# Performance work log

Measured on AMD Instinct MI355X. Metric: run time of the kernel, lower is better.

Reference implementation:

```python
import jax, jax.numpy as jnp
import numpy as np

N_EXPERTS = 64
TOP_K = 4
D_MODEL = 512
D_FF = 2048
B, T = 2, 1024


def setup_inputs() -> dict:
    key = jax.random.key(0)
    k1, k2, k3, k4 = jax.random.split(key, 4)
    x = jax.random.normal(k1, (B, T, D_MODEL), dtype=jnp.float32)
    hex_weights = jax.random.uniform(k2, (B, T, N_EXPERTS), dtype=jnp.float32)
    W_in = jax.random.normal(k3, (N_EXPERTS, D_FF, D_MODEL), dtype=jnp.float32) * (D_MODEL ** -0.5)
    W_out = jax.random.normal(k4, (N_EXPERTS, D_MODEL, D_FF), dtype=jnp.float32) * (D_FF ** -0.5)
    bias_in = jnp.zeros((N_EXPERTS, D_FF), dtype=jnp.float32)
    bias_out = jnp.zeros((N_EXPERTS, D_MODEL), dtype=jnp.float32)
    return {"x": x, "hex_weights": hex_weights, "W_in": W_in, "bias_in": bias_in,
            "W_out": W_out, "bias_out": bias_out}


def reference(x, hex_weights, W_in, bias_in, W_out, bias_out):
    # x: (B,T,D); hex_weights: (B,T,64)
    Bv, Tv, D = x.shape
    N = Bv * Tv
    xf = x.reshape(N, D)
    hw = hex_weights.reshape(N, N_EXPERTS)
    top_w, top_idx = jax.lax.top_k(hw, TOP_K)                 # (N,K)
    top_w = top_w / (jnp.sum(top_w, axis=-1, keepdims=True) + 1e-8)
    # Sparse combine matrix: row n has top_w at selected experts, 0 elsewhere.
    combine = jnp.zeros((N, N_EXPERTS), dtype=x.dtype).at[
        jnp.arange(N)[:, None], top_idx].add(top_w)            # (N,64)
    # Scan over the 64 experts; equivalent math to per-token weight gather,
    # since combine is zero for unselected experts.
    def body(acc, ew):
        Wi, bi, Wo, bo, c = ew                                 # Wi:(d_ff,D), c:(N,)
        h = jax.nn.silu(xf @ Wi.T + bi)                        # (N,d_ff)
        o = h @ Wo.T + bo                                      # (N,D)
        return acc + c[:, None] * o, None
    out, _ = jax.lax.scan(body, jnp.zeros_like(xf),
                          (W_in, bias_in, W_out, bias_out, combine.T))
    return out.reshape(Bv, Tv, D)
```

## Files before the change

kernel.cpp:

```cpp
#include <hip/hip_runtime.h>
#include <hip/hip_bf16.h>
#include <stdint.h>

#define NTOK 2048
#define NE 64
#define TOPK 4
#define DM 512
#define DF 2048
#define TOTSLOT (NTOK*TOPK)

#define BM 192
#define BN 128
#define BK 64
#define GEMM_GRID 1024

typedef __bf16 bf16;
typedef __bf16 bf16x8 __attribute__((ext_vector_type(8)));
typedef __bf16 bf16x4 __attribute__((ext_vector_type(4)));
typedef float  f32x4  __attribute__((ext_vector_type(4)));
typedef short  short8 __attribute__((ext_vector_type(8)));


__global__ void k_route(const float* __restrict__ hw, float* __restrict__ top_w,
                        int* __restrict__ top_idx) {
  int t = blockIdx.x * blockDim.x + threadIdx.x;
  if (t >= NTOK) return;
  const float* r = hw + (size_t)t * NE;
  float rv[NE];
  #pragma unroll
  for (int e = 0; e < NE; ++e) rv[e] = r[e];
  float v[TOPK]; int id[TOPK];
  #pragma unroll
  for (int k = 0; k < TOPK; ++k) {
    float best = -1e30f; int bi = 0;
    #pragma unroll
    for (int e = 0; e < NE; ++e) {
      bool used = false;
      #pragma unroll
      for (int j = 0; j < k; ++j) used |= (id[j] == e);
      if (!used && rv[e] > best) { best = rv[e]; bi = e; }
    }
    v[k] = best; id[k] = bi;
  }
  float den = v[0] + v[1] + v[2] + v[3] + 1e-8f;
  #pragma unroll
  for (int k = 0; k < TOPK; ++k) {
    top_w[t*TOPK + k] = v[k] / den;
    top_idx[t*TOPK + k] = id[k];
  }
}

__global__ __launch_bounds__(256) void k_build(
    const int* __restrict__ top_idx, int* __restrict__ tok,
    int* __restrict__ slot_of, int* __restrict__ offsets_g,
    int* __restrict__ tasklist, int* __restrict__ ntask_g) {
  __shared__ int cnt_s[NE], off_s[NE + 1], fill_s[NE], tpre_s[NE + 1];
  const int tid = threadIdx.x;
  if (tid < NE) { cnt_s[tid] = 0; fill_s[tid] = 0; }
  __syncthreads();
  int ids[TOTSLOT / 256];
  #pragma unroll
  for (int c = 0; c < TOTSLOT / 256; ++c) {
    ids[c] = top_idx[c * 256 + tid];
    atomicAdd(&cnt_s[ids[c]], 1);
  }
  __syncthreads();
  if (tid < 64) {
    int c = cnt_s[tid];
    int inc = c;
    #pragma unroll
    for (int d = 1; d < 64; d <<= 1) {
      int n = __shfl_up(inc, d, 64);
      if (tid >= d) inc += n;
    }
    off_s[tid] = inc - c;
    if (tid == 63) off_s[64] = inc;

    int tc = (c + BM - 1) / BM;
    int tinc = tc;
    #pragma unroll
    for (int d = 1; d < 64; d <<= 1) {
      int n = __shfl_up(tinc, d, 64);
      if (tid >= d) tinc += n;
    }
    tpre_s[tid] = tinc - tc;
    if (tid == 63) tpre_s[64] = tinc;
  }
  __syncthreads();
  #pragma unroll
  for (int c = 0; c < TOTSLOT / 256; ++c) {
    int idx = c * 256 + tid;
    int e = ids[c];
    int pos = off_s[e] + atomicAdd(&fill_s[e], 1);
    tok[pos] = idx >> 2;
    slot_of[idx] = pos;
  }
  if (tid < 64) {
    int tc = (cnt_s[tid] + BM - 1) / BM;
    int base = tpre_s[tid];
    for (int m = 0; m < tc; ++m) tasklist[base + m] = (tid << 8) | m;
    if (tid == 0) *ntask_g = tpre_s[64];
  }
  if (tid <= NE) offsets_g[tid] = off_s[tid];
}

__global__ void k_xcast(const float* __restrict__ x, bf16* __restrict__ xb) {
  int i = blockIdx.x * blockDim.x + threadIdx.x;
  int base = i * 4;
  if (base >= NTOK * DM) return;
  float4 f = *(const float4*)(x + base);
  bf16x4 o;
  o[0] = (bf16)f.x; o[1] = (bf16)f.y; o[2] = (bf16)f.z; o[3] = (bf16)f.w;
  *(bf16x4*)(xb + base) = o;
}


template<int PASS, int KSPLIT>
__global__ __launch_bounds__(512) void k_gemm(
    const float* __restrict__ W, const float* __restrict__ bias,
    const bf16* __restrict__ Asrc, const int* __restrict__ tok,
    const int* __restrict__ offsets,
    const int* __restrict__ tasklist, const int* __restrict__ ntask_g,
    bf16* __restrict__ Hout, float* __restrict__ Oout)
{
  constexpr int KFULL = (PASS == 1) ? DM : DF;
  constexpr int KLOC  = KFULL / KSPLIT;
  constexpr int KT    = KLOC / BK;
  constexpr int NDIM  = (PASS == 1) ? DF : DM;
  constexpr int NT    = NDIM / BN;
  constexpr int NTK   = NT * KSPLIT;

  const int tid = threadIdx.x;
  const int wave = tid >> 6, lane = tid & 63;
  const int wm = wave >> 1, wn = wave & 1;
  const int lrow = lane >> 4, lcol = lane & 15;

  __shared__ bf16 As[BM * BK];
  __shared__ bf16 Bs[BN * BK];

  const int tot = (*ntask_g) * NTK;

  #pragma unroll 1
  for (int tt = blockIdx.x; tt < tot; tt += GEMM_GRID) {
    const int emt   = tt / NTK;
    const int rest  = tt - emt * NTK;
    const int ntile = rest / KSPLIT;
    const int ks    = rest - ntile * KSPLIT;
    const int em    = tasklist[emt];
    const int e     = em >> 8;
    const int mt    = em & 255;
    const int kbase = ks * KLOC;

    const int off = offsets[e];
    const int cnt = offsets[e+1] - off;
    const int rowcount = cnt - mt * BM;

    const bf16* abase[3]; bool aok[3];
    #pragma unroll
    for (int c = 0; c < 3; ++c) {
      int r = (c * 512 + tid) >> 3;
      aok[c] = (r < rowcount);
      int srcrow;
      if (PASS == 1) srcrow = aok[c] ? tok[off + mt*BM + r] : 0;
      else           srcrow = min(off + mt*BM + (aok[c] ? r : 0), TOTSLOT - 1);
      abase[c] = Asrc + (size_t)srcrow * KFULL + kbase + (tid & 7) * 8;
    }
    const int brow = tid >> 2;
    const float* bbase = W + (size_t)e * NDIM * KFULL
                           + (size_t)(ntile*BN + brow) * KFULL + kbase + (tid & 3) * 16;

    f32x4 acc[3][4];
    #pragma unroll
    for (int i = 0; i < 3; ++i)
      #pragma unroll
      for (int j = 0; j < 4; ++j) acc[i][j] = (f32x4)(0.0f);

    #pragma unroll 1
    for (int kt = 0; kt < KT; ++kt) {
      const int k0 = kt * BK;
      short8 areg[3];
      #pragma unroll
      for (int c = 0; c < 3; ++c) {
        if (PASS == 2 || aok[c]) areg[c] = *(const short8*)(abase[c] + k0);
        else                     areg[c] = (short8){0,0,0,0,0,0,0,0};
      }
      float4 breg[4];
      #pragma unroll
      for (int q = 0; q < 4; ++q) breg[q] = *(const float4*)(bbase + k0 + q*4);

      __syncthreads();
      #pragma unroll
      for (int c = 0; c < 3; ++c) {
        int r = (c * 512 + tid) >> 3;
        int u = tid & 7;
        *(short8*)(&As[r*BK + ((u ^ (r & 7)) * 8)]) = areg[c];
      }
      {
        const float* fv = (const float*)breg;
        bf16x8 p0, p1;
        #pragma unroll
        for (int q = 0; q < 8; ++q) { p0[q] = (bf16)fv[q]; p1[q] = (bf16)fv[q+8]; }
        int u0 = (tid & 3) * 2;
        *(bf16x8*)(&Bs[brow*BK + (((u0  ) ^ (brow & 7)) * 8)]) = p0;
        *(bf16x8*)(&Bs[brow*BK + (((u0+1) ^ (brow & 7)) * 8)]) = p1;
      }
      __syncthreads();

      #pragma unroll
      for (int ksub = 0; ksub < 2; ++ksub) {
        const int uu = ksub*4 + lrow;
        bf16x8 af[3], bfr[4];
        #pragma unroll
        for (int i = 0; i < 3; ++i) {
          int m = wm*48 + i*16 + lcol;
          af[i] = *(const bf16x8*)(&As[m*BK + ((uu ^ (m & 7)) * 8)]);
        }
        #pragma unroll
        for (int j = 0; j < 4; ++j) {
          int n = wn*64 + j*16 + lcol;
          bfr[j] = *(const bf16x8*)(&Bs[n*BK + ((uu ^ (n & 7)) * 8)]);
        }
        #pragma unroll
        for (int i = 0; i < 3; ++i)
          #pragma unroll
          for (int j = 0; j < 4; ++j)
            acc[i][j] = __builtin_amdgcn_mfma_f32_16x16x32_bf16(af[i], bfr[j], acc[i][j], 0, 0, 0);
      }
    }

    const int slotbase = off + mt * BM;
    #pragma unroll
    for (int i = 0; i < 3; ++i) {
      const int rbase = wm*48 + i*16 + lrow*4;
      #pragma unroll
      for (int j = 0; j < 4; ++j) {
        const int gcol = ntile*BN + wn*64 + j*16 + lcol;
        const float bv = (PASS == 2 && ks != 0) ? 0.0f : bias[(size_t)e * NDIM + gcol];
        #pragma unroll
        for (int q = 0; q < 4; ++q) {
          const int r = rbase + q;
          if (r < rowcount) {
            float h = acc[i][j][q] + bv;
            if (PASS == 1) {
              float s = h / (1.0f + __expf(-h));
              Hout[(size_t)(slotbase + r) * DF + gcol] = (bf16)s;
            } else {
              Oout[(size_t)ks * TOTSLOT * DM + (size_t)(slotbase + r) * DM + gcol] = h;
            }
          }
        }
      }
    }
    __syncthreads();
  }
}


__global__ void k_combine(const float* __restrict__ O, const float* __restrict__ top_w,
                          const int* __restrict__ slot_of, float* __restrict__ out) {
  int i = blockIdx.x * blockDim.x + threadIdx.x;
  if (i >= NTOK * DM / 4) return;
  int t  = i / (DM / 4);
  int d4 = (i % (DM / 4)) * 4;
  float4 s = {0.f, 0.f, 0.f, 0.f};
  #pragma unroll
  for (int k = 0; k < TOPK; ++k) {
    float w = top_w[t*TOPK + k];
    int  sl = slot_of[t*TOPK + k];
    float sx = 0.f, sy = 0.f, sz = 0.f, sw = 0.f;
    #pragma unroll
    for (int p = 0; p < 4; ++p) {
      float4 o = *(const float4*)(O + (size_t)p * TOTSLOT * DM + (size_t)sl * DM + d4);
      sx += o.x; sy += o.y; sz += o.z; sw += o.w;
    }
    s.x += w * sx; s.y += w * sy; s.z += w * sz; s.w += w * sw;
  }
  *(float4*)(out + (size_t)t * DM + d4) = s;
}


extern "C" void kernel_launch(void* const* d_in, const int* in_sizes, int n_in,
                              void* d_out, int out_size, void* d_ws, size_t ws_size,
                              hipStream_t stream) {
  const float* x        = (const float*)d_in[0];
  const float* hw       = (const float*)d_in[1];
  const float* W_in     = (const float*)d_in[2];
  const float* bias_in  = (const float*)d_in[3];
  const float* W_out    = (const float*)d_in[4];
  const float* bias_out = (const float*)d_in[5];
  float* out = (float*)d_out;

  char* ws = (char*)d_ws;
  int*   offsets  = (int*)  (ws + 0);
  int*   ntask    = (int*)  (ws + 512);
  int*   tasklist = (int*)  (ws + 768);
  int*   top_idx  = (int*)  (ws + 2048);
  float* top_w    = (float*)(ws + 2048 + 32768);
  int*   slot_of  = (int*)  (ws + 2048 + 2*32768);
  int*   tok      = (int*)  (ws + 2048 + 3*32768);
  bf16*  xb       = (bf16*) (ws + 2048 + 4*32768);
  size_t o_xb_end = 2048 + 4*32768 + (size_t)NTOK*DM*2;
  bf16*  H        = (bf16*) (ws + o_xb_end);
  size_t o_H_end  = o_xb_end + (size_t)TOTSLOT*DF*2;
  float* O        = (float*)(ws + o_H_end);

  k_route<<<NTOK/256, 256, 0, stream>>>(hw, top_w, top_idx);
  k_build<<<1, 256, 0, stream>>>(top_idx, tok, slot_of, offsets, tasklist, ntask);
  k_xcast<<<(NTOK*DM/4)/256, 256, 0, stream>>>(x, xb);

  k_gemm<1,1><<<GEMM_GRID, 512, 0, stream>>>(W_in, bias_in, xb, tok, offsets,
                                             tasklist, ntask, H, nullptr);
  k_gemm<2,4><<<GEMM_GRID, 512, 0, stream>>>(W_out, bias_out, H, nullptr, offsets,
                                             tasklist, ntask, nullptr, O);

  k_combine<<<(NTOK*DM/4)/256, 256, 0, stream>>>(O, top_w, slot_of, out);
}
```

Measured before the change: 201.2 us.

## Prefetch next K-tile into registers during MFMA and group pass-2 tiles per XCD

The GEMM main loop now issues global loads for the next K-tile before computing the current one, using two register buffers so memory latency overlaps MFMA work. Pass-2 tile scheduling is remapped so blocks landing on the same XCD (tt&7) share a (task, k-split) group across N tiles, aiming for better L2 reuse of A rows. Launch bounds add a min-blocks hint of 4. The extra register buffers raise register pressure, and the hint may force spills. The double-step loop assumes KT is even.

```diff
diff --git a/kernel.cpp b/kernel.cpp
--- a/kernel.cpp
+++ b/kernel.cpp
@@ -116,7 +116,7 @@
 
 
 template<int PASS, int KSPLIT>
-__global__ __launch_bounds__(512) void k_gemm(
+__global__ __launch_bounds__(512, 4) void k_gemm(
     const float* __restrict__ W, const float* __restrict__ bias,
     const bf16* __restrict__ Asrc, const int* __restrict__ tok,
     const int* __restrict__ offsets,
@@ -128,7 +128,6 @@
   constexpr int KT    = KLOC / BK;
   constexpr int NDIM  = (PASS == 1) ? DF : DM;
   constexpr int NT    = NDIM / BN;
-  constexpr int NTK   = NT * KSPLIT;
 
   const int tid = threadIdx.x;
   const int wave = tid >> 6, lane = tid & 63;
@@ -138,17 +137,26 @@
   __shared__ bf16 As[BM * BK];
   __shared__ bf16 Bs[BN * BK];
 
-  const int tot = (*ntask_g) * NTK;
+  const int ntask = *ntask_g;
+  const int NG  = ntask * KSPLIT;
+  const int GD  = (NG + 7) / 8;
+  const int tot = (PASS == 1) ? ntask * NT : 8 * GD * NT;
 
   #pragma unroll 1
   for (int tt = blockIdx.x; tt < tot; tt += GEMM_GRID) {
-    const int emt   = tt / NTK;
-    const int rest  = tt - emt * NTK;
-    const int ntile = rest / KSPLIT;
-    const int ks    = rest - ntile * KSPLIT;
-    const int em    = tasklist[emt];
-    const int e     = em >> 8;
-    const int mt    = em & 255;
+    int taskIdx, ntile, ks;
+    if (PASS == 1) {
+      taskIdx = tt / NT; ntile = tt % NT; ks = 0;
+    } else {
+      const int xcd = tt & 7, slot = tt >> 3;
+      const int g = (slot / NT) * 8 + xcd;
+      if (g >= NG) continue;
+      ntile = slot % NT;
+      taskIdx = g / KSPLIT; ks = g % KSPLIT;
+    }
+    const int em = tasklist[taskIdx];
+    const int e  = em >> 8;
+    const int mt = em & 255;
     const int kbase = ks * KLOC;
 
     const int off = offsets[e];
@@ -169,43 +177,40 @@
     const float* bbase = W + (size_t)e * NDIM * KFULL
                            + (size_t)(ntile*BN + brow) * KFULL + kbase + (tid & 3) * 16;
 
-    f32x4 acc[3][4];
-    #pragma unroll
-    for (int i = 0; i < 3; ++i)
-      #pragma unroll
-      for (int j = 0; j < 4; ++j) acc[i][j] = (f32x4)(0.0f);
-
-    #pragma unroll 1
-    for (int kt = 0; kt < KT; ++kt) {
-      const int k0 = kt * BK;
-      short8 areg[3];
+    auto LOADA = [&](short8 (&ar)[3], int kt) {
       #pragma unroll
       for (int c = 0; c < 3; ++c) {
-        if (PASS == 2 || aok[c]) areg[c] = *(const short8*)(abase[c] + k0);
-        else                     areg[c] = (short8){0,0,0,0,0,0,0,0};
+        if (PASS == 2 || aok[c]) ar[c] = *(const short8*)(abase[c] + kt*BK);
+        else                     ar[c] = (short8){0,0,0,0,0,0,0,0};
       }
-      float4 breg[4];
-      #pragma unroll
-      for (int q = 0; q < 4; ++q) breg[q] = *(const float4*)(bbase + k0 + q*4);
-
-      __syncthreads();
+    };
+    auto LOADB = [&](float4 (&br)[4], int kt) {
+      #pragma unroll
+      for (int q = 0; q < 4; ++q) br[q] = *(const float4*)(bbase + kt*BK + q*4);
+    };
+    auto WRITE = [&](short8 (&ar)[3], float4 (&br)[4]) {
       #pragma unroll
       for (int c = 0; c < 3; ++c) {
         int r = (c * 512 + tid) >> 3;
         int u = tid & 7;
-        *(short8*)(&As[r*BK + ((u ^ (r & 7)) * 8)]) = areg[c];
+        *(short8*)(&As[r*BK + ((u ^ (r & 7)) * 8)]) = ar[c];
       }
-      {
-        const float* fv = (const float*)breg;
-        bf16x8 p0, p1;
-        #pragma unroll
-        for (int q = 0; q < 8; ++q) { p0[q] = (bf16)fv[q]; p1[q] = (bf16)fv[q+8]; }
-        int u0 = (tid & 3) * 2;
-        *(bf16x8*)(&Bs[brow*BK + (((u0  ) ^ (brow & 7)) * 8)]) = p0;
-        *(bf16x8*)(&Bs[brow*BK + (((u0+1) ^ (brow & 7)) * 8)]) = p1;
-      }
-      __syncthreads();
-
+      const float* fv = (const float*)br;
+      bf16x8 p0, p1;
+      #pragma unroll
+      for (int q = 0; q < 8; ++q) { p0[q] = (bf16)fv[q]; p1[q] = (bf16)fv[q+8]; }
+      int u0 = (tid & 3) * 2;
+      *(bf16x8*)(&Bs[brow*BK + (((u0  ) ^ (brow & 7)) * 8)]) = p0;
+      *(bf16x8*)(&Bs[brow*BK + (((u0+1) ^ (brow & 7)) * 8)]) = p1;
+    };
+
+    f32x4 acc[3][4];
+    #pragma unroll
+    for (int i = 0; i < 3; ++i)
+      #pragma unroll
+      for (int j = 0; j < 4; ++j) acc[i][j] = (f32x4)(0.0f);
+
+    auto COMPUTE = [&]() {
       #pragma unroll
       for (int ksub = 0; ksub < 2; ++ksub) {
         const int uu = ksub*4 + lrow;
@@ -226,6 +231,22 @@
           for (int j = 0; j < 4; ++j)
             acc[i][j] = __builtin_amdgcn_mfma_f32_16x16x32_bf16(af[i], bfr[j], acc[i][j], 0, 0, 0);
       }
+    };
+
+    short8 a0[3], a1[3]; float4 b0[4], b1[4];
+    LOADA(a0, 0); LOADB(b0, 0);
+    #pragma unroll 1
+    for (int kt = 0; kt < KT; kt += 2) {
+      __syncthreads();
+      WRITE(a0, b0);
+      __syncthreads();
+      LOADA(a1, kt + 1); LOADB(b1, kt + 1);
+      COMPUTE();
+      __syncthreads();
+      WRITE(a1, b1);
+      __syncthreads();
+      if (kt + 2 < KT) { LOADA(a0, kt + 2); LOADB(b0, kt + 2); }
+      COMPUTE();
     }
 
     const int slotbase = off + mt * BM;
```

Measured after the change: 349.9 us. 73.9% more time.

## Fuse weighted combine into second GEMM epilogue via atomic adds

Applied to the files above, without the earlier changes.

Removes the separate combine kernel and the split-K partial output buffer. The down-projection epilogue now scales each result by its routing weight and atomically adds it into the zeroed output at the owning token's row. Per-slot weights are precomputed in the build kernel. This saves writing and re-reading the large intermediate buffer. In exchange it costs a memset and many scattered float atomics (split-K by four, top-4), and the summation order becomes nondeterministic.

```diff
diff --git a/kernel.cpp b/kernel.cpp
--- a/kernel.cpp
+++ b/kernel.cpp
@@ -51,7 +51,8 @@
 }
 
 __global__ __launch_bounds__(256) void k_build(
-    const int* __restrict__ top_idx, int* __restrict__ tok,
+    const int* __restrict__ top_idx, const float* __restrict__ top_w,
+    int* __restrict__ tok, float* __restrict__ wslot,
     int* __restrict__ slot_of, int* __restrict__ offsets_g,
     int* __restrict__ tasklist, int* __restrict__ ntask_g) {
   __shared__ int cnt_s[NE], off_s[NE + 1], fill_s[NE], tpre_s[NE + 1];
@@ -93,6 +94,7 @@
     int e = ids[c];
     int pos = off_s[e] + atomicAdd(&fill_s[e], 1);
     tok[pos] = idx >> 2;
+    wslot[pos] = top_w[idx];
     slot_of[idx] = pos;
   }
   if (tid < 64) {
@@ -119,9 +121,9 @@
 __global__ __launch_bounds__(512) void k_gemm(
     const float* __restrict__ W, const float* __restrict__ bias,
     const bf16* __restrict__ Asrc, const int* __restrict__ tok,
-    const int* __restrict__ offsets,
+    const float* __restrict__ wslot, const int* __restrict__ offsets,
     const int* __restrict__ tasklist, const int* __restrict__ ntask_g,
-    bf16* __restrict__ Hout, float* __restrict__ Oout)
+    bf16* __restrict__ Hout, float* __restrict__ out)
 {
   constexpr int KFULL = (PASS == 1) ? DM : DF;
   constexpr int KLOC  = KFULL / KSPLIT;
@@ -245,7 +247,8 @@
               float s = h / (1.0f + __expf(-h));
               Hout[(size_t)(slotbase + r) * DF + gcol] = (bf16)s;
             } else {
-              Oout[(size_t)ks * TOTSLOT * DM + (size_t)(slotbase + r) * DM + gcol] = h;
+              const int slot = slotbase + r;
+              atomicAdd(&out[(size_t)tok[slot] * DM + gcol], wslot[slot] * h);
             }
           }
         }
@@ -253,29 +256,6 @@
     }
     __syncthreads();
   }
-}
-
-
-__global__ void k_combine(const float* __restrict__ O, const float* __restrict__ top_w,
-                          const int* __restrict__ slot_of, float* __restrict__ out) {
-  int i = blockIdx.x * blockDim.x + threadIdx.x;
-  if (i >= NTOK * DM / 4) return;
-  int t  = i / (DM / 4);
-  int d4 = (i % (DM / 4)) * 4;
-  float4 s = {0.f, 0.f, 0.f, 0.f};
-  #pragma unroll
-  for (int k = 0; k < TOPK; ++k) {
-    float w = top_w[t*TOPK + k];
-    int  sl = slot_of[t*TOPK + k];
-    float sx = 0.f, sy = 0.f, sz = 0.f, sw = 0.f;
-    #pragma unroll
-    for (int p = 0; p < 4; ++p) {
-      float4 o = *(const float4*)(O + (size_t)p * TOTSLOT * DM + (size_t)sl * DM + d4);
-      sx += o.x; sy += o.y; sz += o.z; sw += o.w;
-    }
-    s.x += w * sx; s.y += w * sy; s.z += w * sz; s.w += w * sw;
-  }
-  *(float4*)(out + (size_t)t * DM + d4) = s;
 }
 
 
@@ -298,20 +278,19 @@
   float* top_w    = (float*)(ws + 2048 + 32768);
   int*   slot_of  = (int*)  (ws + 2048 + 2*32768);
   int*   tok      = (int*)  (ws + 2048 + 3*32768);
-  bf16*  xb       = (bf16*) (ws + 2048 + 4*32768);
-  size_t o_xb_end = 2048 + 4*32768 + (size_t)NTOK*DM*2;
+  float* wslot    = (float*)(ws + 2048 + 4*32768);
+  bf16*  xb       = (bf16*) (ws + 2048 + 5*32768);
+  size_t o_xb_end = 2048 + 5*32768 + (size_t)NTOK*DM*2;
   bf16*  H        = (bf16*) (ws + o_xb_end);
-  size_t o_H_end  = o_xb_end + (size_t)TOTSLOT*DF*2;
-  float* O        = (float*)(ws + o_H_end);
 
   k_route<<<NTOK/256, 256, 0, stream>>>(hw, top_w, top_idx);
-  k_build<<<1, 256, 0, stream>>>(top_idx, tok, slot_of, offsets, tasklist, ntask);
+  k_build<<<1, 256, 0, stream>>>(top_idx, top_w, tok, wslot, slot_of,
+                                 offsets, tasklist, ntask);
   k_xcast<<<(NTOK*DM/4)/256, 256, 0, stream>>>(x, xb);
-
-  k_gemm<1,1><<<GEMM_GRID, 512, 0, stream>>>(W_in, bias_in, xb, tok, offsets,
-                                             tasklist, ntask, H, nullptr);
-  k_gemm<2,4><<<GEMM_GRID, 512, 0, stream>>>(W_out, bias_out, H, nullptr, offsets,
-                                             tasklist, ntask, nullptr, O);
-
-  k_combine<<<(NTOK*DM/4)/256, 256, 0, stream>>>(O, top_w, slot_of, out);
-}
+  hipMemsetAsync(d_out, 0, (size_t)out_size * sizeof(float), stream);
+
+  k_gemm<1,1><<<GEMM_GRID, 512, 0, stream>>>(W_in, bias_in, xb, tok, nullptr,
+                                             offsets, tasklist, ntask, H, nullptr);
+  k_gemm<2,4><<<GEMM_GRID, 512, 0, stream>>>(W_out, bias_out, H, tok, wslot,
+                                             offsets, tasklist, ntask, nullptr, out);
+}
```

New measurement: 231.1 us. 1.15x slower.
